# Performance work log

Measured on AMD Instinct MI355X. Metric: run time of the kernel, lower is better.

Reference implementation:

```python
import jax, jax.numpy as jnp
import numpy as np

N_NODES = 100000
N_EDGES = 1600000
D = 128
N_LAYERS = 4
N_GRAPHS = 512


def setup_inputs() -> dict:
    key = jax.random.key(0)
    ks = jax.random.split(key, 12)
    x = jax.random.normal(ks[0], (N_NODES, D), dtype=jnp.float32)
    edge_index = jax.random.randint(ks[1], (2, N_EDGES), 0, N_NODES, dtype=jnp.int64)
    batch = jnp.sort(jax.random.randint(ks[2], (N_NODES,), 0, N_GRAPHS, dtype=jnp.int64))
    scale = 1.0 / np.sqrt(D)
    Ws = jax.random.normal(ks[3], (N_LAYERS, D, D), dtype=jnp.float32) * scale
    bs = jnp.zeros((N_LAYERS, D), dtype=jnp.float32)
    mlp_w1 = jax.random.normal(ks[4], (D, 100), dtype=jnp.float32) * scale
    mlp_b1 = jnp.zeros((100,), dtype=jnp.float32)
    mlp_w2 = jax.random.normal(ks[5], (100, 4), dtype=jnp.float32) * (1.0 / np.sqrt(100.0))
    mlp_b2 = jnp.zeros((4,), dtype=jnp.float32)
    return {"x": x, "Ws": Ws, "bs": bs, "mlp_w1": mlp_w1, "mlp_b1": mlp_b1,
            "mlp_w2": mlp_w2, "mlp_b2": mlp_b2, "edge_index": edge_index, "batch": batch}


def _gcn_conv(x, W, b, row, col, norm):
    # x: [N, Din]; W: [Din, Dout]. PyG GCNConv: linear, then normalized scatter-add.
    xw = x @ W                                # [N, Dout]
    msg = xw[row] * norm[:, None]             # gather at source nodes [E', Dout]
    out = jax.ops.segment_sum(msg, col, num_segments=N_NODES)
    return out + b


def reference(x, Ws, bs, mlp_w1, mlp_b1, mlp_w2, mlp_b2, edge_index, batch):
    # Add self-loops and compute symmetric normalization (once; shared by all layers).
    loop = jnp.arange(N_NODES, dtype=edge_index.dtype)
    row = jnp.concatenate([edge_index[0], loop])  # source
    col = jnp.concatenate([edge_index[1], loop])  # target
    deg = jax.ops.segment_sum(jnp.ones_like(col, dtype=x.dtype), col, num_segments=N_NODES)
    dinv = jnp.where(deg > 0, jax.lax.rsqrt(deg), 0.0)
    norm = dinv[row] * dinv[col]              # [E']

    h = x
    for i in range(N_LAYERS - 1):
        # dropout is identity in eval mode
        h = _gcn_conv(h, Ws[i], bs[i], row, col, norm)
        h = jax.nn.relu(h)
    h = _gcn_conv(h, Ws[-1], bs[-1], row, col, norm)

    # global mean pool over graphs
    sums = jax.ops.segment_sum(h, batch, num_segments=N_GRAPHS)
    counts = jax.ops.segment_sum(jnp.ones((N_NODES,), dtype=h.dtype), batch, num_segments=N_GRAPHS)
    pooled = sums / jnp.maximum(counts, 1.0)[:, None]  # [G, D]

    # MLP head: D -> 100 -> 4 (relu between, dropout identity in eval)
    hid = jax.nn.relu(pooled @ mlp_w1 + mlp_b1)
    pred = hid @ mlp_w2 + mlp_b2
    return pred
```

## Files before the change

### kernel.cpp

```cpp
#include <hip/hip_runtime.h>

#define N_NODES  100000
#define N_EDGES  1600000
#define DIM      128
#define N_GRAPHS 512

#define BW       512
#define NBUCK    ((N_NODES + BW - 1) / BW)
#define CAP      12288
#define NB_CHUNK 4096

typedef short  bf16x8 __attribute__((ext_vector_type(8)));
typedef float  f32x4  __attribute__((ext_vector_type(4)));

__device__ inline ushort f2bf(float f) {
    union { float f; unsigned u; } v; v.f = f;
    unsigned r = v.u + 0x7FFFu + ((v.u >> 16) & 1u);
    return (ushort)(r >> 16);
}
__device__ inline float bf2f_lo(unsigned u) { union { unsigned u; float f; } v; v.u = u << 16; return v.f; }
__device__ inline float bf2f_hi(unsigned u) { union { unsigned u; float f; } v; v.u = u & 0xFFFF0000u; return v.f; }


__global__ __launch_bounds__(256) void cvt_x(const float* __restrict__ x,
                                             const float* __restrict__ dinv,
                                             ushort* __restrict__ xb) {
    int i = (blockIdx.x * 256 + threadIdx.x) * 4;
    float d = dinv[i >> 7];
    float4 v = *(const float4*)(x + i);
    ushort4 o;
    o.x = f2bf(v.x * d); o.y = f2bf(v.y * d); o.z = f2bf(v.z * d); o.w = f2bf(v.w * d);
    *(ushort4*)(xb + i) = o;
}

__global__ __launch_bounds__(256) void cvt_w(const float* __restrict__ Ws,
                                             ushort* __restrict__ WT) {
    int idx = blockIdx.x * 256 + threadIdx.x;
    int L = idx >> 14, n = (idx >> 7) & 127, k = idx & 127;
    WT[idx] = f2bf(Ws[(L << 14) + (k << 7) + n]);
}


__global__ __launch_bounds__(256) void initb_kernel(int* __restrict__ bfill,
                                                    int* __restrict__ csr) {
    int t = threadIdx.x;
    if (t < NBUCK) bfill[t] = t * CAP;
    if (t == 255) csr[N_NODES] = N_EDGES;
}

__global__ __launch_bounds__(1024) void bin_kernel(const int* __restrict__ row,
                                                   const int* __restrict__ col,
                                                   int* __restrict__ bfill,
                                                   unsigned* __restrict__ tmp) {
    __shared__ unsigned s_val[NB_CHUNK];
    __shared__ int s_dst[NB_CHUNK];
    __shared__ int s_hist[256], s_scan[256];
    __shared__ int s_excl[NBUCK], s_base[NBUCK], s_cur[NBUCK];
    int t = threadIdx.x;
    int e0 = blockIdx.x * NB_CHUNK;

    if (t < 256) s_hist[t] = 0;
    __syncthreads();
#pragma unroll
    for (int k = 0; k < 4; ++k) {
        int e = e0 + t + k * 1024;
        if (e < N_EDGES) atomicAdd(&s_hist[col[e] >> 9], 1);
    }
    __syncthreads();
    int h = 0;
    if (t < 256) { h = s_hist[t]; s_scan[t] = h; }
    __syncthreads();
    for (int o = 1; o < 256; o <<= 1) {
        int u = 0;
        if (t < 256 && t >= o) u = s_scan[t - o];
        __syncthreads();
        if (t < 256) s_scan[t] += u;
        __syncthreads();
    }
    if (t < NBUCK) {
        int ex = s_scan[t] - h;
        s_excl[t] = ex;
        s_cur[t]  = ex;
        s_base[t] = atomicAdd(&bfill[t], h);
    }
    __syncthreads();
#pragma unroll
    for (int k = 0; k < 4; ++k) {
        int e = e0 + t + k * 1024;
        if (e < N_EDGES) {
            int r = row[e], c = col[e];
            int b = c >> 9;
            int p = atomicAdd(&s_cur[b], 1);
            int dst = s_base[b] + (p - s_excl[b]);
            int lim = (b + 1) * CAP;
            if (dst >= lim) dst = lim - 1;
            s_val[p] = ((unsigned)(c & (BW - 1)) << 17) | (unsigned)r;
            s_dst[p] = dst;
        }
    }
    __syncthreads();
    int sc = N_EDGES - e0; if (sc > NB_CHUNK) sc = NB_CHUNK;
#pragma unroll
    for (int k = 0; k < 4; ++k) {
        int j = t + k * 1024;
        if (j < sc) tmp[s_dst[j]] = s_val[j];
    }
}

__global__ __launch_bounds__(256) void bscan_kernel(const int* __restrict__ bfill,
                                                    int* __restrict__ bbase) {
    __shared__ int s[256];
    int t = threadIdx.x;
    int cnt = 0;
    if (t < NBUCK) {
        cnt = bfill[t] - t * CAP;
        if (cnt > CAP) cnt = CAP;
    }
    s[t] = cnt;
    __syncthreads();
    for (int o = 1; o < 256; o <<= 1) {
        int u = (t >= o) ? s[t - o] : 0;
        __syncthreads();
        s[t] += u;
        __syncthreads();
    }
    if (t < NBUCK) bbase[t] = s[t] - cnt;
}

__global__ __launch_bounds__(1024) void sort_kernel(const unsigned* __restrict__ tmp,
                                                    const int* __restrict__ bfill,
                                                    const int* __restrict__ bbase,
                                                    int* __restrict__ csr,
                                                    float* __restrict__ dinv,
                                                    int* __restrict__ ssrc) {
    __shared__ int s_cnt[BW];
    __shared__ int s_pair[256];
    __shared__ int s_off[BW];
    __shared__ int s_cur[BW];
    __shared__ int s_stage[CAP];
    int b = blockIdx.x, t = threadIdx.x;
    int wbeg = b * BW;
    int wn = N_NODES - wbeg; if (wn > BW) wn = BW;
    int nE = bfill[b] - b * CAP; if (nE > CAP) nE = CAP;
    const unsigned* T = tmp + (size_t)b * CAP;
    int base = bbase[b];

    for (int i = t; i < BW; i += 1024) s_cnt[i] = 0;
    __syncthreads();
    for (int i = t; i < nE; i += 1024) atomicAdd(&s_cnt[T[i] >> 17], 1);
    __syncthreads();
    int a0 = 0, a1 = 0;
    if (t < 256) { a0 = s_cnt[2 * t]; a1 = s_cnt[2 * t + 1]; s_pair[t] = a0 + a1; }
    __syncthreads();
    for (int o = 1; o < 256; o <<= 1) {
        int u = 0;
        if (t < 256 && t >= o) u = s_pair[t - o];
        __syncthreads();
        if (t < 256) s_pair[t] += u;
        __syncthreads();
    }
    if (t < 256) {
        int pre = s_pair[t] - (a0 + a1);
        s_off[2 * t] = pre;      s_off[2 * t + 1] = pre + a0;
        s_cur[2 * t] = pre;      s_cur[2 * t + 1] = pre + a0;
    }
    __syncthreads();
    for (int i = t; i < wn; i += 1024) {
        csr[wbeg + i]  = base + s_off[i];
        dinv[wbeg + i] = rsqrtf((float)(s_cnt[i] + 1));
    }
    for (int i = t; i < nE; i += 1024) {
        unsigned v = T[i];
        int p = atomicAdd(&s_cur[v >> 17], 1);
        s_stage[p] = (int)(v & 0x1FFFFu);
    }
    __syncthreads();
    for (int i = t; i < nE; i += 1024) ssrc[base + i] = s_stage[i];
}

__global__ __launch_bounds__(256) void bounds_kernel(const int* __restrict__ batch,
                                                     int* __restrict__ gstart) {
    int i = blockIdx.x * 256 + threadIdx.x;
    if (i >= N_NODES) return;
    int b  = batch[i];
    int bp = (i == 0) ? -1 : batch[i - 1];
    for (int g = bp + 1; g <= b; ++g) gstart[g] = i;
    if (i == N_NODES - 1) {
        for (int g = b + 1; g <= N_GRAPHS; ++g) gstart[g] = N_NODES;
    }
}

#define ACC8(vv) do { \
    acc[0] += bf2f_lo((vv).x); acc[1] += bf2f_hi((vv).x); \
    acc[2] += bf2f_lo((vv).y); acc[3] += bf2f_hi((vv).y); \
    acc[4] += bf2f_lo((vv).z); acc[5] += bf2f_hi((vv).z); \
    acc[6] += bf2f_lo((vv).w); acc[7] += bf2f_hi((vv).w); } while (0)

__global__ __launch_bounds__(512) void layer_kernel(const ushort* __restrict__ g,
                                                    const ushort* __restrict__ WT,
                                                    const float* __restrict__ bias,
                                                    const float* __restrict__ dinv,
                                                    const int* __restrict__ csr,
                                                    const int* __restrict__ ssrc,
                                                    ushort* __restrict__ out,
                                                    int mode) {
    __shared__ ushort sW[128 * 128];
    __shared__ ushort sA[8][16 * 128];
    int t = threadIdx.x;
    int m0blk = blockIdx.x * 128;

    {
#pragma unroll
        for (int j = 0; j < 4; ++j) {
            int idx = t + j * 512;
            int r = idx >> 4, c = idx & 15;
            uint4 v = *(const uint4*)(WT + (size_t)r * 128 + c * 8);
            *(uint4*)(sW + r * 128 + ((c + r) & 15) * 8) = v;
        }
    }
    __syncthreads();

    int wv   = t >> 6;
    int lane = t & 63;
    int q    = lane >> 4;
    int l    = lane & 15;
    int mw   = m0blk + wv * 16;
    ushort* sAw = sA[wv];
    const uint4* hp = (const uint4*)g;

#pragma unroll 1
    for (int i = 0; i < 4; ++i) {
        int row  = q * 4 + i;
        int node = mw + row;
        float acc[8];
#pragma unroll
        for (int z = 0; z < 8; ++z) acc[z] = 0.f;
        if (node < N_NODES) {
            uint4 v = hp[(size_t)node * 16 + l];
            acc[0] = bf2f_lo(v.x); acc[1] = bf2f_hi(v.x);
            acc[2] = bf2f_lo(v.y); acc[3] = bf2f_hi(v.y);
            acc[4] = bf2f_lo(v.z); acc[5] = bf2f_hi(v.z);
            acc[6] = bf2f_lo(v.w); acc[7] = bf2f_hi(v.w);
            int e = csr[node], end = csr[node + 1];
            for (; e + 3 < end; e += 4) {
                int s0 = ssrc[e], s1 = ssrc[e + 1], s2 = ssrc[e + 2], s3 = ssrc[e + 3];
                uint4 v0 = hp[(size_t)s0 * 16 + l];
                uint4 v1 = hp[(size_t)s1 * 16 + l];
                uint4 v2 = hp[(size_t)s2 * 16 + l];
                uint4 v3 = hp[(size_t)s3 * 16 + l];
                ACC8(v0); ACC8(v1); ACC8(v2); ACC8(v3);
            }
            if (e + 1 < end) {
                int s0 = ssrc[e], s1 = ssrc[e + 1];
                uint4 v0 = hp[(size_t)s0 * 16 + l];
                uint4 v1 = hp[(size_t)s1 * 16 + l];
                ACC8(v0); ACC8(v1);
                e += 2;
            }
            if (e < end) {
                int s = ssrc[e];
                uint4 v1 = hp[(size_t)s * 16 + l];
                ACC8(v1);
            }
            float d = dinv[node];
#pragma unroll
            for (int z = 0; z < 8; ++z) acc[z] *= d;
        }
        uint4 ov;
        ov.x = (uint)f2bf(acc[0]) | ((uint)f2bf(acc[1]) << 16);
        ov.y = (uint)f2bf(acc[2]) | ((uint)f2bf(acc[3]) << 16);
        ov.z = (uint)f2bf(acc[4]) | ((uint)f2bf(acc[5]) << 16);
        ov.w = (uint)f2bf(acc[6]) | ((uint)f2bf(acc[7]) << 16);
        *(uint4*)(sAw + row * 128 + ((l + row) & 15) * 8) = ov;
    }

    f32x4 facc[8];
#pragma unroll
    for (int n = 0; n < 8; ++n) facc[n] = (f32x4){0.f, 0.f, 0.f, 0.f};
#pragma unroll
    for (int ki = 0; ki < 4; ++ki) {
        int ca = ki * 4 + q;
        bf16x8 a = *(const bf16x8*)(sAw + l * 128 + ((ca + l) & 15) * 8);
#pragma unroll
        for (int n = 0; n < 8; ++n) {
            int rB = n * 16 + l;
            bf16x8 b = *(const bf16x8*)(sW + rB * 128 + ((ca + rB) & 15) * 8);
            facc[n] = __builtin_amdgcn_mfma_f32_16x16x32_bf16(a, b, facc[n], 0, 0, 0);
        }
    }

    {
        int lr0 = q * 4;
        float sc[4];
#pragma unroll
        for (int r = 0; r < 4; ++r) {
            int m = mw + lr0 + r;
            sc[r] = (mode && m < N_NODES) ? dinv[m] : 1.0f;
        }
#pragma unroll
        for (int n = 0; n < 8; ++n) {
            int col = n * 16 + l;
            float bv = bias[col];
            int c = col >> 3;
#pragma unroll
            for (int r = 0; r < 4; ++r) {
                int lr = lr0 + r;
                float v = facc[n][r] + bv;
                if (mode) v = fmaxf(v, 0.f) * sc[r];
                sAw[lr * 128 + ((c + lr) & 15) * 8 + (col & 7)] = f2bf(v);
            }
        }
    }
#pragma unroll
    for (int j = 0; j < 4; ++j) {
        int idx = lane + j * 64;
        int lr = idx >> 4, c = idx & 15;
        int m = mw + lr;
        if (m < N_NODES) {
            uint4 v = *(const uint4*)(sAw + lr * 128 + ((c + lr) & 15) * 8);
            *(uint4*)(out + (size_t)m * 128 + c * 8) = v;
        }
    }
}


__global__ __launch_bounds__(256) void pool_mlp(const ushort* __restrict__ h,
                                                const int* __restrict__ gstart,
                                                const float* __restrict__ w1,
                                                const float* __restrict__ b1,
                                                const float* __restrict__ w2,
                                                const float* __restrict__ b2,
                                                float* __restrict__ out) {
    __shared__ float part[4][128];
    __shared__ float mean[128];
    __shared__ float hid[100];
    int g = blockIdx.x;
    int s = gstart[g], e2 = gstart[g + 1];
    int p     = threadIdx.x & 63;
    int which = threadIdx.x >> 6;
    const uint* hu = (const uint*)h;

    float a0 = 0.f, a1 = 0.f;
    for (int n = s + which; n < e2; n += 4) {
        uint v = hu[(size_t)n * 64 + p];
        a0 += bf2f_lo(v);
        a1 += bf2f_hi(v);
    }
    part[which][2 * p]     = a0;
    part[which][2 * p + 1] = a1;
    __syncthreads();
    if (which == 0) {
        float c = fmaxf((float)(e2 - s), 1.0f);
        mean[2 * p]     = (part[0][2 * p] + part[1][2 * p] + part[2][2 * p] + part[3][2 * p]) / c;
        mean[2 * p + 1] = (part[0][2 * p + 1] + part[1][2 * p + 1] + part[2][2 * p + 1] + part[3][2 * p + 1]) / c;
    }
    __syncthreads();
    int t = threadIdx.x;
    if (t < 100) {
        float s1 = b1[t];
        for (int k = 0; k < 128; ++k) s1 = fmaf(mean[k], w1[k * 100 + t], s1);
        hid[t] = fmaxf(s1, 0.f);
    }
    __syncthreads();
    if (t < 4) {
        float s2 = b2[t];
        for (int j = 0; j < 100; ++j) s2 = fmaf(hid[j], w2[j * 4 + t], s2);
        out[(size_t)g * 4 + t] = s2;
    }
}


extern "C" void kernel_launch(void* const* d_in, const int* in_sizes, int n_in,
                              void* d_out, int out_size, void* d_ws, size_t ws_size,
                              hipStream_t stream) {
    const float* x   = (const float*)d_in[0];
    const float* Ws  = (const float*)d_in[1];
    const float* bs  = (const float*)d_in[2];
    const float* w1  = (const float*)d_in[3];
    const float* b1  = (const float*)d_in[4];
    const float* w2  = (const float*)d_in[5];
    const float* b2  = (const float*)d_in[6];
    const int*   ei  = (const int*)d_in[7];
    const int*   bat = (const int*)d_in[8];
    float* outp = (float*)d_out;

    char* p = (char*)d_ws;
    auto take = [&](size_t bytes) -> void* {
        void* r = (void*)p;
        p += (bytes + 255) & ~(size_t)255;
        return r;
    };
    int*      csr    = (int*)take((size_t)(N_NODES + 1) * 4);
    float*    dinv   = (float*)take((size_t)N_NODES * 4);
    int*      bfill  = (int*)take((size_t)NBUCK * 4);
    int*      bbase  = (int*)take((size_t)NBUCK * 4);
    unsigned* tmp    = (unsigned*)take((size_t)NBUCK * CAP * 4);
    int*      ssrc   = (int*)take((size_t)N_EDGES * 4);
    ushort*   xb     = (ushort*)take((size_t)N_NODES * 128 * 2);
    ushort*   hbA    = (ushort*)take((size_t)N_NODES * 128 * 2);
    ushort*   hbB    = (ushort*)take((size_t)N_NODES * 128 * 2);
    ushort*   WT     = (ushort*)take((size_t)4 * 128 * 128 * 2);
    int*      gstart = (int*)take((size_t)(N_GRAPHS + 1) * 4);

    const int* row = ei;
    const int* col = ei + N_EDGES;

    initb_kernel<<<1, 256, 0, stream>>>(bfill, csr);
    bin_kernel<<<(N_EDGES + NB_CHUNK - 1) / NB_CHUNK, 1024, 0, stream>>>(row, col, bfill, tmp);
    bscan_kernel<<<1, 256, 0, stream>>>(bfill, bbase);
    sort_kernel<<<NBUCK, 1024, 0, stream>>>(tmp, bfill, bbase, csr, dinv, ssrc);
    cvt_x<<<12500, 256, 0, stream>>>(x, dinv, xb);
    cvt_w<<<256, 256, 0, stream>>>(Ws, WT);
    bounds_kernel<<<(N_NODES + 255) / 256, 256, 0, stream>>>(bat, gstart);

    const ushort* hin = xb;
    ushort* hout = hbA;
    for (int L = 0; L < 4; ++L) {
        layer_kernel<<<(N_NODES + 127) / 128, 512, 0, stream>>>(
            hin, WT + (size_t)L * 128 * 128, bs + (size_t)L * 128, dinv,
            csr, ssrc, hout, (L < 3) ? 1 : 0);
        hin = hout;
        hout = (hout == hbA) ? hbB : hbA;
    }
    pool_mlp<<<N_GRAPHS, 256, 0, stream>>>(hin, gstart, w1, b1, w2, b2, outp);
}
```

Before: 459.0 us.

## Gather neighbor rows directly into MFMA A-fragment registers, drop sA staging

Each lane now owns one node (row l) and gathers the four 16-byte column chunks that match its MFMA A-fragment layout. The aggregated row is packed straight into bf16x8 registers, so the per-wave shared-memory staging tile is gone. The output epilogue also writes 2-byte elements straight to global memory instead of restaging through LDS for 16-byte stores. This trades the old four-rows-per-lane serial gather, where 16 lanes shared one row, for one row per lane with more loads in flight. The risks are more register pressure, divergent degree loops across the 16 lanes, and uncoalesced narrow stores.

```diff
diff --git a/kernel.cpp b/kernel.cpp
--- a/kernel.cpp
+++ b/kernel.cpp
@@ -190,11 +190,11 @@
     }
 }
 
-#define ACC8(vv) do { \
-    acc[0] += bf2f_lo((vv).x); acc[1] += bf2f_hi((vv).x); \
-    acc[2] += bf2f_lo((vv).y); acc[3] += bf2f_hi((vv).y); \
-    acc[4] += bf2f_lo((vv).z); acc[5] += bf2f_hi((vv).z); \
-    acc[6] += bf2f_lo((vv).w); acc[7] += bf2f_hi((vv).w); } while (0)
+#define ACCK(ki, vv) do { \
+    acc[ki][0] += bf2f_lo((vv).x); acc[ki][1] += bf2f_hi((vv).x); \
+    acc[ki][2] += bf2f_lo((vv).y); acc[ki][3] += bf2f_hi((vv).y); \
+    acc[ki][4] += bf2f_lo((vv).z); acc[ki][5] += bf2f_hi((vv).z); \
+    acc[ki][6] += bf2f_lo((vv).w); acc[ki][7] += bf2f_hi((vv).w); } while (0)
 
 __global__ __launch_bounds__(512) void layer_kernel(const ushort* __restrict__ g,
                                                     const ushort* __restrict__ WT,
@@ -205,7 +205,6 @@
                                                     ushort* __restrict__ out,
                                                     int mode) {
     __shared__ ushort sW[128 * 128];
-    __shared__ ushort sA[8][16 * 128];
     int t = threadIdx.x;
     int m0blk = blockIdx.x * 128;
 
@@ -225,53 +224,46 @@
     int q    = lane >> 4;
     int l    = lane & 15;
     int mw   = m0blk + wv * 16;
-    ushort* sAw = sA[wv];
+    int node = mw + l;
+    int nclamp = (node < N_NODES) ? node : (N_NODES - 1);
     const uint4* hp = (const uint4*)g;
 
-#pragma unroll 1
-    for (int i = 0; i < 4; ++i) {
-        int row  = q * 4 + i;
-        int node = mw + row;
-        float acc[8];
-#pragma unroll
-        for (int z = 0; z < 8; ++z) acc[z] = 0.f;
-        if (node < N_NODES) {
-            uint4 v = hp[(size_t)node * 16 + l];
-            acc[0] = bf2f_lo(v.x); acc[1] = bf2f_hi(v.x);
-            acc[2] = bf2f_lo(v.y); acc[3] = bf2f_hi(v.y);
-            acc[4] = bf2f_lo(v.z); acc[5] = bf2f_hi(v.z);
-            acc[6] = bf2f_lo(v.w); acc[7] = bf2f_hi(v.w);
-            int e = csr[node], end = csr[node + 1];
-            for (; e + 3 < end; e += 4) {
-                int s0 = ssrc[e], s1 = ssrc[e + 1], s2 = ssrc[e + 2], s3 = ssrc[e + 3];
-                uint4 v0 = hp[(size_t)s0 * 16 + l];
-                uint4 v1 = hp[(size_t)s1 * 16 + l];
-                uint4 v2 = hp[(size_t)s2 * 16 + l];
-                uint4 v3 = hp[(size_t)s3 * 16 + l];
-                ACC8(v0); ACC8(v1); ACC8(v2); ACC8(v3);
-            }
-            if (e + 1 < end) {
-                int s0 = ssrc[e], s1 = ssrc[e + 1];
-                uint4 v0 = hp[(size_t)s0 * 16 + l];
-                uint4 v1 = hp[(size_t)s1 * 16 + l];
-                ACC8(v0); ACC8(v1);
-                e += 2;
-            }
-            if (e < end) {
-                int s = ssrc[e];
-                uint4 v1 = hp[(size_t)s * 16 + l];
-                ACC8(v1);
-            }
-            float d = dinv[node];
-#pragma unroll
-            for (int z = 0; z < 8; ++z) acc[z] *= d;
-        }
-        uint4 ov;
-        ov.x = (uint)f2bf(acc[0]) | ((uint)f2bf(acc[1]) << 16);
-        ov.y = (uint)f2bf(acc[2]) | ((uint)f2bf(acc[3]) << 16);
-        ov.z = (uint)f2bf(acc[4]) | ((uint)f2bf(acc[5]) << 16);
-        ov.w = (uint)f2bf(acc[6]) | ((uint)f2bf(acc[7]) << 16);
-        *(uint4*)(sAw + row * 128 + ((l + row) & 15) * 8) = ov;
+    float acc[4][8];
+#pragma unroll
+    for (int a2 = 0; a2 < 4; ++a2)
+#pragma unroll
+        for (int z = 0; z < 8; ++z) acc[a2][z] = 0.f;
+
+    {
+        const uint4* rp = hp + (size_t)nclamp * 16 + q;
+        uint4 v0 = rp[0], v1 = rp[4], v2 = rp[8], v3 = rp[12];
+        ACCK(0, v0); ACCK(1, v1); ACCK(2, v2); ACCK(3, v3);
+    }
+    int e = csr[nclamp], end = csr[nclamp + 1];
+    for (; e + 1 < end; e += 2) {
+        int s0 = ssrc[e], s1 = ssrc[e + 1];
+        const uint4* r0 = hp + (size_t)s0 * 16 + q;
+        const uint4* r1 = hp + (size_t)s1 * 16 + q;
+        uint4 x0 = r0[0], x1 = r0[4], x2 = r0[8], x3 = r0[12];
+        uint4 y0 = r1[0], y1 = r1[4], y2 = r1[8], y3 = r1[12];
+        ACCK(0, x0); ACCK(1, x1); ACCK(2, x2); ACCK(3, x3);
+        ACCK(0, y0); ACCK(1, y1); ACCK(2, y2); ACCK(3, y3);
+    }
+    if (e < end) {
+        int s0 = ssrc[e];
+        const uint4* r0 = hp + (size_t)s0 * 16 + q;
+        uint4 x0 = r0[0], x1 = r0[4], x2 = r0[8], x3 = r0[12];
+        ACCK(0, x0); ACCK(1, x1); ACCK(2, x2); ACCK(3, x3);
+    }
+    float d = dinv[nclamp];
+
+    bf16x8 afrag[4];
+#pragma unroll
+    for (int ki = 0; ki < 4; ++ki) {
+        union { ushort u[8]; bf16x8 v; } pk;
+#pragma unroll
+        for (int z = 0; z < 8; ++z) pk.u[z] = f2bf(acc[ki][z] * d);
+        afrag[ki] = pk.v;
     }
 
     f32x4 facc[8];
@@ -280,45 +272,33 @@
 #pragma unroll
     for (int ki = 0; ki < 4; ++ki) {
         int ca = ki * 4 + q;
-        bf16x8 a = *(const bf16x8*)(sAw + l * 128 + ((ca + l) & 15) * 8);
 #pragma unroll
         for (int n = 0; n < 8; ++n) {
             int rB = n * 16 + l;
             bf16x8 b = *(const bf16x8*)(sW + rB * 128 + ((ca + rB) & 15) * 8);
-            facc[n] = __builtin_amdgcn_mfma_f32_16x16x32_bf16(a, b, facc[n], 0, 0, 0);
+            facc[n] = __builtin_amdgcn_mfma_f32_16x16x32_bf16(afrag[ki], b, facc[n], 0, 0, 0);
         }
     }
 
-    {
-        int lr0 = q * 4;
-        float sc[4];
+    int orow = mw + q * 4;
+    float sc[4];
+#pragma unroll
+    for (int r = 0; r < 4; ++r) {
+        int m = orow + r;
+        sc[r] = (mode && m < N_NODES) ? dinv[m] : 1.0f;
+    }
+#pragma unroll
+    for (int n = 0; n < 8; ++n) {
+        int col = n * 16 + l;
+        float bv = bias[col];
 #pragma unroll
         for (int r = 0; r < 4; ++r) {
-            int m = mw + lr0 + r;
-            sc[r] = (mode && m < N_NODES) ? dinv[m] : 1.0f;
-        }
-#pragma unroll
-        for (int n = 0; n < 8; ++n) {
-            int col = n * 16 + l;
-            float bv = bias[col];
-            int c = col >> 3;
-#pragma unroll
-            for (int r = 0; r < 4; ++r) {
-                int lr = lr0 + r;
+            int m = orow + r;
+            if (m < N_NODES) {
                 float v = facc[n][r] + bv;
                 if (mode) v = fmaxf(v, 0.f) * sc[r];
-                sAw[lr * 128 + ((c + lr) & 15) * 8 + (col & 7)] = f2bf(v);
+                out[(size_t)m * 128 + col] = f2bf(v);
             }
-        }
-    }
-#pragma unroll
-    for (int j = 0; j < 4; ++j) {
-        int idx = lane + j * 64;
-        int lr = idx >> 4, c = idx & 15;
-        int m = mw + lr;
-        if (m < N_NODES) {
-            uint4 v = *(const uint4*)(sAw + lr * 128 + ((c + lr) & 15) * 8);
-            *(uint4*)(out + (size_t)m * 128 + c * 8) = v;
         }
     }
 }
```

Result: slower. 536.4 us (+16.9%).

## Build MFMA A fragments via ds_bpermute and drop per-wave LDS staging

Applied to the files above, without the earlier changes.

Removes the 32KB per-block sA shared-memory staging buffer. Each wave now keeps its aggregated rows in registers and builds the MFMA A operands with ds_bpermute lane shuffles. The epilogue writes bf16 results straight to global memory as scalar 2-byte stores instead of re-staging through LDS for 16-byte coalesced stores. This lowers LDS use per block, which may allow more resident blocks, but costs many bpermute ops and produces narrow, less coalesced global writes.

```diff
diff --git a/kernel.cpp b/kernel.cpp
--- a/kernel.cpp
+++ b/kernel.cpp
@@ -205,7 +205,6 @@
                                                     ushort* __restrict__ out,
                                                     int mode) {
     __shared__ ushort sW[128 * 128];
-    __shared__ ushort sA[8][16 * 128];
     int t = threadIdx.x;
     int m0blk = blockIdx.x * 128;
 
@@ -225,9 +224,9 @@
     int q    = lane >> 4;
     int l    = lane & 15;
     int mw   = m0blk + wv * 16;
-    ushort* sAw = sA[wv];
     const uint4* hp = (const uint4*)g;
 
+    uint P[4][4];
 #pragma unroll 1
     for (int i = 0; i < 4; ++i) {
         int row  = q * 4 + i;
@@ -266,12 +265,29 @@
 #pragma unroll
             for (int z = 0; z < 8; ++z) acc[z] *= d;
         }
-        uint4 ov;
-        ov.x = (uint)f2bf(acc[0]) | ((uint)f2bf(acc[1]) << 16);
-        ov.y = (uint)f2bf(acc[2]) | ((uint)f2bf(acc[3]) << 16);
-        ov.z = (uint)f2bf(acc[4]) | ((uint)f2bf(acc[5]) << 16);
-        ov.w = (uint)f2bf(acc[6]) | ((uint)f2bf(acc[7]) << 16);
-        *(uint4*)(sAw + row * 128 + ((l + row) & 15) * 8) = ov;
+#pragma unroll
+        for (int w = 0; w < 4; ++w)
+            P[i][w] = (uint)f2bf(acc[2 * w]) | ((uint)f2bf(acc[2 * w + 1]) << 16);
+    }
+
+    int sel = l & 3;
+    int srcq16 = (l >> 2) * 16;
+    bf16x8 afrag[4];
+#pragma unroll
+    for (int ki = 0; ki < 4; ++ki) {
+        int idx4 = (srcq16 + 4 * ki + q) * 4;
+        union { uint u[4]; bf16x8 v; } pk;
+#pragma unroll
+        for (int w = 0; w < 4; ++w) {
+            uint t0 = (uint)__builtin_amdgcn_ds_bpermute(idx4, (int)P[0][w]);
+            uint t1 = (uint)__builtin_amdgcn_ds_bpermute(idx4, (int)P[1][w]);
+            uint t2 = (uint)__builtin_amdgcn_ds_bpermute(idx4, (int)P[2][w]);
+            uint t3 = (uint)__builtin_amdgcn_ds_bpermute(idx4, (int)P[3][w]);
+            uint f01 = (sel & 1) ? t1 : t0;
+            uint f23 = (sel & 1) ? t3 : t2;
+            pk.u[w] = (sel & 2) ? f23 : f01;
+        }
+        afrag[ki] = pk.v;
     }
 
     f32x4 facc[8];
@@ -280,45 +296,33 @@
 #pragma unroll
     for (int ki = 0; ki < 4; ++ki) {
         int ca = ki * 4 + q;
-        bf16x8 a = *(const bf16x8*)(sAw + l * 128 + ((ca + l) & 15) * 8);
 #pragma unroll
         for (int n = 0; n < 8; ++n) {
             int rB = n * 16 + l;
             bf16x8 b = *(const bf16x8*)(sW + rB * 128 + ((ca + rB) & 15) * 8);
-            facc[n] = __builtin_amdgcn_mfma_f32_16x16x32_bf16(a, b, facc[n], 0, 0, 0);
-        }
-    }
-
-    {
-        int lr0 = q * 4;
-        float sc[4];
+            facc[n] = __builtin_amdgcn_mfma_f32_16x16x32_bf16(afrag[ki], b, facc[n], 0, 0, 0);
+        }
+    }
+
+    int orow = mw + q * 4;
+    float sc[4];
+#pragma unroll
+    for (int r = 0; r < 4; ++r) {
+        int m = orow + r;
+        sc[r] = (mode && m < N_NODES) ? dinv[m] : 1.0f;
+    }
+#pragma unroll
+    for (int n = 0; n < 8; ++n) {
+        int col = n * 16 + l;
+        float bv = bias[col];
 #pragma unroll
         for (int r = 0; r < 4; ++r) {
-            int m = mw + lr0 + r;
-            sc[r] = (mode && m < N_NODES) ? dinv[m] : 1.0f;
-        }
-#pragma unroll
-        for (int n = 0; n < 8; ++n) {
-            int col = n * 16 + l;
-            float bv = bias[col];
-            int c = col >> 3;
-#pragma unroll
-            for (int r = 0; r < 4; ++r) {
-                int lr = lr0 + r;
+            int m = orow + r;
+            if (m < N_NODES) {
                 float v = facc[n][r] + bv;
                 if (mode) v = fmaxf(v, 0.f) * sc[r];
-                sAw[lr * 128 + ((c + lr) & 15) * 8 + (col & 7)] = f2bf(v);
+                out[(size_t)m * 128 + col] = f2bf(v);
             }
-        }
-    }
-#pragma unroll
-    for (int j = 0; j < 4; ++j) {
-        int idx = lane + j * 64;
-        int lr = idx >> 4, c = idx & 15;
-        int m = mw + lr;
-        if (m < N_NODES) {
-            uint4 v = *(const uint4*)(sAw + lr * 128 + ((c + lr) & 15) * 8);
-            *(uint4*)(out + (size_t)m * 128 + c * 8) = v;
         }
     }
 }
```

New measurement: 518.4 us. +12.9%, slower.
